# Kernel optimization log

Hardware: AMD Instinct MI355X
Metric: run time of the kernel (lower is better)

## Reference

```python
import jax, jax.numpy as jnp
import numpy as np

B, T, D = 2, 2048, 1024
NH, DH = 16, 64  # inner = NH*DH = D
SCALE_INIT = 0.02


def setup_inputs() -> dict:
    key = jax.random.key(0)
    kx, kq, kk, kv, ko = jax.random.split(key, 5)
    return {
        "x": jax.random.normal(kx, (B, T, D), dtype=jnp.float32),
        "Wq": jax.random.normal(kq, (D, NH * DH), dtype=jnp.float32) * SCALE_INIT,
        "Wk": jax.random.normal(kk, (D, NH * DH), dtype=jnp.float32) * SCALE_INIT,
        "Wv": jax.random.normal(kv, (D, NH * DH), dtype=jnp.float32) * SCALE_INIT,
        "Wo": jax.random.normal(ko, (NH * DH, D), dtype=jnp.float32) * SCALE_INIT,
    }


def reference(x, Wq, Wk, Wv, Wo):
    # x: (B, T, D)
    b, t, _ = x.shape

    def split_heads(h):
        # (B, T, NH*DH) -> (B, NH, T, DH)
        return h.reshape(b, t, NH, DH).transpose(0, 2, 1, 3)

    q = split_heads(x @ Wq)
    k = split_heads(x @ Wk)
    v = split_heads(x @ Wv)

    scale = jnp.asarray(1.0 / np.sqrt(DH), dtype=x.dtype)
    # The per-chunk loop in the original is mathematically equivalent to
    # full causal attention: each query row attends to keys with k_pos <= q_pos.
    scores = jnp.einsum("bhqd,bhkd->bhqk", q, k) * scale  # (B, NH, T, T)
    causal_mask = jnp.arange(t)[None, :] > jnp.arange(t)[:, None]  # k_pos > q_pos
    scores = jnp.where(causal_mask, -jnp.inf, scores)
    attn = jax.nn.softmax(scores, axis=-1)
    attn = jnp.nan_to_num(attn)  # matches torch.nan_to_num (no fully-masked rows in causal case)
    o = jnp.einsum("bhqk,bhkd->bhqd", attn, v)  # (B, NH, T, DH)
    o = o.transpose(0, 2, 1, 3).reshape(b, t, NH * DH)  # merge heads
    return o @ Wo  # (B, T, D)
```

## Files before the change

### kernel.cpp

```cpp
#include <hip/hip_runtime.h>
#include <hip/hip_bf16.h>
#include <string.h>

#define Bsz 2
#define Tsz 2048
#define Dsz 1024
#define NHsz 16
#define Msz (Bsz*Tsz)

typedef unsigned short bfu;
typedef __attribute__((ext_vector_type(8))) short short8;
typedef __attribute__((ext_vector_type(4))) short short4v;
typedef __attribute__((ext_vector_type(4))) float floatx4;

__device__ __forceinline__ bfu f2bf(float f) {
  unsigned int u = __builtin_bit_cast(unsigned int, f);
  u += 0x7fffu + ((u >> 16) & 1u);
  return (bfu)(u >> 16);
}

__device__ __forceinline__ float fexp2(float x) {
#if __has_builtin(__builtin_amdgcn_exp2f)
  return __builtin_amdgcn_exp2f(x);
#else
  return exp2f(x);
#endif
}

__device__ __forceinline__ short4v pack4bf(float a, float b, float c_, float d) {
  __hip_bfloat162 h01 = __float22bfloat162_rn(make_float2(a, b));
  __hip_bfloat162 h23 = __float22bfloat162_rn(make_float2(c_, d));
  uint2 uu;
  memcpy(&uu.x, &h01, 4);
  memcpy(&uu.y, &h23, 4);
  return __builtin_bit_cast(short4v, uu);
}

__device__ __forceinline__ short8 pack8bf(float4 a, float4 b) {
  __hip_bfloat162 h0 = __float22bfloat162_rn(make_float2(a.x, a.y));
  __hip_bfloat162 h1 = __float22bfloat162_rn(make_float2(a.z, a.w));
  __hip_bfloat162 h2 = __float22bfloat162_rn(make_float2(b.x, b.y));
  __hip_bfloat162 h3 = __float22bfloat162_rn(make_float2(b.z, b.w));
  uint4 u;
  memcpy(&u.x, &h0, 4); memcpy(&u.y, &h1, 4);
  memcpy(&u.z, &h2, 4); memcpy(&u.w, &h3, 4);
  return __builtin_bit_cast(short8, u);
}

__device__ __forceinline__ void async16(const void* g, void* l) {
  void* gnc = (void*)g;
  __builtin_amdgcn_global_load_lds((__attribute__((address_space(1))) void*)gnc,
                                   (__attribute__((address_space(3))) void*)l,
                                   16, 0, 0);
}

__global__ __launch_bounds__(256) void transpose_w(const float* __restrict__ W0, const float* __restrict__ W1,
                                                   const float* __restrict__ W2, const float* __restrict__ W3,
                                                   bfu* __restrict__ wt,
                                                   const float* __restrict__ x, bfu* __restrict__ xb) {
  if (blockIdx.z == 4) {
    const int bf = (int)blockIdx.y * 32 + (int)blockIdx.x;
    const size_t i = ((size_t)bf * 256 + threadIdx.y * 32 + threadIdx.x) * 16;
    float4 a0 = *(const float4*)(x + i),     a1 = *(const float4*)(x + i + 4);
    float4 b0 = *(const float4*)(x + i + 8), b1 = *(const float4*)(x + i + 12);
    *(short8*)(xb + i)     = pack8bf(a0, a1);
    *(short8*)(xb + i + 8) = pack8bf(b0, b1);
    return;
  }
  __shared__ float tile[32][33];
  const float* W = blockIdx.z == 0 ? W0 : blockIdx.z == 1 ? W1 : blockIdx.z == 2 ? W2 : W3;
  const float s = (blockIdx.z == 0) ? 0.18033688011112042f : 1.0f;
  bfu* WT = wt + (size_t)blockIdx.z * Dsz * Dsz;
  int tx = threadIdx.x, ty = threadIdx.y;
  int kb = blockIdx.y * 32, nb = blockIdx.x * 32;
#pragma unroll
  for (int i = 0; i < 4; ++i)
    tile[ty + i*8][tx] = W[(size_t)(kb + ty + i*8) * Dsz + nb + tx];
  __syncthreads();
#pragma unroll
  for (int i = 0; i < 4; ++i)
    WT[(size_t)(nb + ty + i*8) * Dsz + kb + tx] = f2bf(tile[tx][ty + i*8] * s);
}

template <bool F32OUT, int NT>
__global__ __launch_bounds__(256) void gemm128(const bfu* __restrict__ Ain, const bfu* __restrict__ Bt0,
                                               void* __restrict__ C0, int K, int N,
                                               size_t strideB, size_t strideC) {
  constexpr int NJ = NT / 32;
  const int tid = threadIdx.x, wave = tid >> 6, lane = tid & 63;
  const int g = lane >> 4, c = lane & 15;
  const int m0 = blockIdx.y * 128, n0 = blockIdx.x * NT;
  const bfu* Bt = Bt0 + strideB * blockIdx.z;
  __shared__ bfu smem[2][4096 + NT * 32];
  floatx4 acc[4][NJ] = {};
  const int srow = lane >> 2;
  const int scol = (((lane & 3) ^ ((lane >> 3) & 3)) << 3);
  const bfu* gB = Bt + (size_t)(n0 + srow) * K + scol;
  const bfu* gA = Ain + (size_t)(m0 + srow) * K + scol;
  const int wm = (wave >> 1) * 64, wn = (wave & 1) * (NT / 2);
  const int roct = (g ^ ((c >> 1) & 3)) << 3;

#define STAGE_G(buf, k0)                                                        \
  {                                                                             \
    _Pragma("unroll")                                                           \
    for (int cc = 0; cc < 2; ++cc) {                                            \
      const int chunk = wave * 2 + cc;                                          \
      async16(gA + (size_t)chunk * 16 * K + (k0), &smem[buf][chunk * 512]);     \
    }                                                                           \
    _Pragma("unroll")                                                           \
    for (int cc = 0; cc < NT / 64; ++cc) {                                      \
      const int chunk = wave * (NT / 64) + cc;                                  \
      async16(gB + (size_t)chunk * 16 * K + (k0), &smem[buf][4096 + chunk * 512]); \
    }                                                                           \
  }

  const int NK = K / 32;
  STAGE_G(0, 0);
  for (int t = 0; t < NK; ++t) {
    const int cur = t & 1;
    if (t + 1 < NK) {
      STAGE_G(cur ^ 1, (t + 1) * 32);
      if (NT == 128) asm volatile("s_waitcnt vmcnt(4)" ::: "memory");
      else           asm volatile("s_waitcnt vmcnt(3)" ::: "memory");
    } else {
      asm volatile("s_waitcnt vmcnt(0)" ::: "memory");
    }
    __builtin_amdgcn_s_barrier();
    asm volatile("" ::: "memory");

    const bfu* AsC = &smem[cur][0];
    const bfu* BsC = &smem[cur][4096];
    short8 afr[4], bfr[NJ];
#pragma unroll
    for (int i = 0; i < 4; ++i) afr[i] = *(const short8*)&AsC[(wm + i*16 + c) * 32 + roct];
#pragma unroll
    for (int j = 0; j < NJ; ++j) bfr[j] = *(const short8*)&BsC[(wn + j*16 + c) * 32 + roct];
#pragma unroll
    for (int i = 0; i < 4; ++i)
#pragma unroll
      for (int j = 0; j < NJ; ++j)
        acc[i][j] = __builtin_amdgcn_mfma_f32_16x16x32_bf16(afr[i], bfr[j], acc[i][j], 0, 0, 0);

    asm volatile("" ::: "memory");
    __builtin_amdgcn_s_barrier();
    asm volatile("" ::: "memory");
  }
#undef STAGE_G

  const bool vtrans = (!F32OUT) && (NT == 128) && (blockIdx.z == 2);
  if (vtrans) {
    bfu* sm = &smem[0][0];
    bfu* vtp = (bfu*)C0 + (size_t)2 * strideC;
#pragma unroll
    for (int p = 0; p < 2; ++p) {
      __syncthreads();
      if ((wave & 1) == p) {
#pragma unroll
        for (int i = 0; i < 4; ++i)
#pragma unroll
          for (int j = 0; j < NJ; ++j) {
            const int nl = j*16 + c;
            const int mg = ((wm + i*16) >> 3) + (g >> 1);
            const int phys = nl * 128 + ((mg ^ (nl & 15)) << 3) + ((g & 1) << 2);
            *(short4v*)&sm[phys] = pack4bf(acc[i][j][0], acc[i][j][1],
                                           acc[i][j][2], acc[i][j][3]);
          }
      }
      __syncthreads();
      const int h_ = (n0 + p * 64) >> 6;
      bfu* dst = vtp + ((size_t)((m0 >> 11) * 16 + h_) * 64) * Tsz + (m0 & 2047);
#pragma unroll
      for (int s = 0; s < 4; ++s) {
        const int nl = s * 16 + (tid >> 4);
        const int me = (tid & 15) << 3;
        const int phys = nl * 128 + (((me >> 3) ^ (nl & 15)) << 3);
        *(short8*)&dst[(size_t)nl * Tsz + me] = *(const short8*)&sm[phys];
      }
    }
    return;
  }

#pragma unroll
  for (int i = 0; i < 4; ++i) {
#pragma unroll
    for (int j = 0; j < NJ; ++j) {
      const int m = m0 + wm + i*16 + g*4;
      const int n = n0 + wn + j*16 + c;
#pragma unroll
      for (int r = 0; r < 4; ++r) {
        float v = acc[i][j][r];
        if (F32OUT) ((float*)C0)[(size_t)(m + r) * N + n] = v;
        else        ((bfu*)C0)[strideC * blockIdx.z + (size_t)(m + r) * N + n] = f2bf(v);
      }
    }
  }
}

__global__ __launch_bounds__(256, 4) void attn_kernel(const bfu* __restrict__ qkv,
                                                      float* __restrict__ op0,
                                                      float* __restrict__ op1,
                                                      float2* __restrict__ ml) {
  const int tid = threadIdx.x, wave = tid >> 6, lane = tid & 63;
  const int g = (lane >> 4) & 3, c = lane & 15, c7 = c & 7;

  const int flat = (int)blockIdx.y * 32 + (int)blockIdx.x;
  const int xcd = flat & 7, r_ = flat >> 3;
  const int ksplit = r_ & 1;
  const int s = (r_ >> 1) & 3, j0 = r_ >> 3;
  const int bh = xcd * 4 + s;
  const int b = bh >> 4, h = bh & 15;

  const size_t hbq = (size_t)b * Tsz * Dsz + h * 64;
  const bfu* Qp = qkv + hbq;
  const bfu* Kp = qkv + (size_t)Msz * Dsz + hbq;
  const bfu* Vt = qkv + (size_t)2 * Msz * Dsz + (size_t)bh * 64 * Tsz;
  float* op = ksplit ? op1 : op0;

  __shared__ bfu Ks[2][64 * 64];
  __shared__ bfu Vs[2][64 * 64];

  const int srow8 = lane >> 3;
  const int soff = ((lane & 7) ^ srow8) << 3;
  const floatx4 z4 = {0.0f, 0.0f, 0.0f, 0.0f};

  for (int hf = 0; hf < 2; ++hf) {
    const int j = hf ? (31 - j0) : j0;
    const int qw = j * 64 + wave * 16;

    short8 bq[2];
#pragma unroll
    for (int kk = 0; kk < 2; ++kk)
      bq[kk] = *(const short8*)(Qp + (size_t)(qw + c) * Dsz + kk * 32 + g * 8);

    floatx4 acc[4] = {};
    float mi = -3.0e38f, li = 0.0f;

    if (ksplit <= j) {
      const bfu* kpp[2]; const bfu* vpp[2];
#pragma unroll
      for (int cc = 0; cc < 2; ++cc) {
        const int ch = wave * 2 + cc;
        kpp[cc] = Kp + (size_t)(ksplit * 64 + ch * 8 + srow8) * Dsz + soff;
        vpp[cc] = Vt + (size_t)(ch * 8 + srow8) * Tsz + ksplit * 64 + soff;
      }

#pragma unroll
      for (int cc = 0; cc < 2; ++cc) {
        const int ch = wave * 2 + cc;
        async16(kpp[cc], &Ks[0][ch * 512]);
        async16(vpp[cc], &Vs[0][ch * 512]);
        kpp[cc] += (size_t)128 * Dsz;
        vpp[cc] += 128;
      }

      int cur = 0;
      for (int kt = ksplit; kt <= j; kt += 2) {
        if (kt + 2 <= j) {
#pragma unroll
          for (int cc = 0; cc < 2; ++cc) {
            const int ch = wave * 2 + cc;
            async16(kpp[cc], &Ks[cur ^ 1][ch * 512]);
            async16(vpp[cc], &Vs[cur ^ 1][ch * 512]);
            kpp[cc] += (size_t)128 * Dsz;
            vpp[cc] += 128;
          }
          asm volatile("s_waitcnt vmcnt(4)" ::: "memory");
        } else {
          asm volatile("s_waitcnt vmcnt(0)" ::: "memory");
        }
        __builtin_amdgcn_s_barrier();
        asm volatile("" ::: "memory");

        const bfu* KsC = &Ks[cur][0];
        const bfu* VsC = &Vs[cur][0];

        floatx4 st[4];
        __builtin_amdgcn_s_setprio(1);
#pragma unroll
        for (int mk = 0; mk < 4; ++mk) {
          const short8 kf = *(const short8*)&KsC[(mk * 16 + c) * 64 + ((g ^ c7) << 3)];
          st[mk] = __builtin_amdgcn_mfma_f32_16x16x32_bf16(kf, bq[0], z4, 0, 0, 0);
        }
#pragma unroll
        for (int mk = 0; mk < 4; ++mk) {
          const short8 kf = *(const short8*)&KsC[(mk * 16 + c) * 64 + (((4 + g) ^ c7) << 3)];
          st[mk] = __builtin_amdgcn_mfma_f32_16x16x32_bf16(kf, bq[1], st[mk], 0, 0, 0);
        }
        __builtin_amdgcn_s_setprio(0);

        if (kt == j) {
#pragma unroll
          for (int mk = 0; mk < 4; ++mk) {
            const int keyb = kt * 64 + mk * 16 + g * 4;
#pragma unroll
            for (int r = 0; r < 4; ++r)
              if (keyb + r > qw + c) st[mk][r] = -1.0e38f;
          }
        }

        float mloc = -3.0e38f;
#pragma unroll
        for (int mk = 0; mk < 4; ++mk)
          mloc = fmaxf(mloc, fmaxf(fmaxf(st[mk][0], st[mk][1]),
                                   fmaxf(st[mk][2], st[mk][3])));
        const bool resc = !__all(mloc <= mi + 8.0f);
        if (resc) {
          float mr = fmaxf(mloc, __shfl_xor(mloc, 16));
          mr = fmaxf(mr, __shfl_xor(mr, 32));
          const float mnew = fmaxf(mi, mr);
          const float alpha = fexp2(mi - mnew);
          li *= alpha;
          mi = mnew;
          float al[4];
#pragma unroll
          for (int rr = 0; rr < 4; ++rr) al[rr] = __shfl(alpha, (lane & 48) | (g * 4 + rr));
#pragma unroll
          for (int nd = 0; nd < 4; ++nd)
#pragma unroll
            for (int rr = 0; rr < 4; ++rr) acc[nd][rr] *= al[rr];
        }
        short4v pa[4];
#pragma unroll
        for (int mk = 0; mk < 4; ++mk) {
          const float p0 = fexp2(st[mk][0] - mi);
          const float p1 = fexp2(st[mk][1] - mi);
          const float p2 = fexp2(st[mk][2] - mi);
          const float p3 = fexp2(st[mk][3] - mi);
          li += (p0 + p1) + (p2 + p3);
          pa[mk] = pack4bf(p0, p1, p2, p3);
        }

        __builtin_amdgcn_s_setprio(1);
#pragma unroll
        for (int mk = 0; mk < 4; ++mk)
#pragma unroll
          for (int nd = 0; nd < 4; ++nd) {
            const short4v vf = *(const short4v*)&VsC[(nd * 16 + c) * 64 +
                ((((mk << 1) + (g >> 1)) ^ c7) << 3) + ((g & 1) << 2)];
            acc[nd] = __builtin_amdgcn_mfma_f32_16x16x16bf16_1k(pa[mk], vf, acc[nd], 0, 0, 0);
          }
        __builtin_amdgcn_s_setprio(0);

        asm volatile("" ::: "memory");
        __builtin_amdgcn_s_barrier();
        asm volatile("" ::: "memory");
        cur ^= 1;
      }
    }

    float lt = li;
    lt += __shfl_xor(lt, 16);
    lt += __shfl_xor(lt, 32);
#pragma unroll
    for (int rr = 0; rr < 4; ++rr) {
      const float lr = __shfl(lt, (lane & 48) | (g * 4 + rr));
      const float inv = lr > 0.0f ? 1.0f / lr : 0.0f;
#pragma unroll
      for (int nd = 0; nd < 4; ++nd)
        op[(size_t)(b * Tsz + qw + g * 4 + rr) * Dsz + h * 64 + nd * 16 + c] =
            acc[nd][rr] * inv;
    }
    if (lane < 16)
      ml[(size_t)ksplit * 65536 + bh * 2048 + qw + c] = make_float2(mi, lt);
  }
}

__global__ __launch_bounds__(256) void merge_split(const float* __restrict__ o0,
                                                   const float* __restrict__ o1,
                                                   const float2* __restrict__ ml,
                                                   bfu* __restrict__ ob) {
  const int idx = blockIdx.x * 256 + threadIdx.x;
  const int row = idx >> 7, ch = idx & 127;
  const int b = row >> 11, q = row & 2047;
  const int bh = b * 16 + (ch >> 3);
  const float2 a0 = ml[bh * 2048 + q];
  const float2 a1 = ml[65536 + bh * 2048 + q];
  const float M = fmaxf(a0.x, a1.x);
  const float w0 = fexp2(a0.x - M) * a0.y;
  const float w1 = fexp2(a1.x - M) * a1.y;
  const float inv = 1.0f / (w0 + w1);
  const float u0 = w0 * inv, u1 = w1 * inv;
  const size_t off = (size_t)row * 1024 + ch * 8;
  float4 p0 = *(const float4*)(o0 + off), q0 = *(const float4*)(o0 + off + 4);
  float4 p1 = *(const float4*)(o1 + off), q1 = *(const float4*)(o1 + off + 4);
  float4 ra, rb;
  ra.x = u0*p0.x + u1*p1.x; ra.y = u0*p0.y + u1*p1.y;
  ra.z = u0*p0.z + u1*p1.z; ra.w = u0*p0.w + u1*p1.w;
  rb.x = u0*q0.x + u1*q1.x; rb.y = u0*q0.y + u1*q1.y;
  rb.z = u0*q0.z + u1*q1.z; rb.w = u0*q0.w + u1*q1.w;
  *(short8*)(ob + off) = pack8bf(ra, rb);
}

extern "C" void kernel_launch(void* const* d_in, const int* in_sizes, int n_in,
                              void* d_out, int out_size, void* d_ws, size_t ws_size,
                              hipStream_t stream) {
  const float* x  = (const float*)d_in[0];
  const float* Wq = (const float*)d_in[1];
  const float* Wk = (const float*)d_in[2];
  const float* Wv = (const float*)d_in[3];
  const float* Wo = (const float*)d_in[4];
  float* out = (float*)d_out;

  bfu* wt    = (bfu*)d_ws;
  bfu* qkv   = wt + (size_t)4 * Dsz * Dsz;
  bfu* obuf  = qkv + (size_t)3 * Msz * Dsz;
  float* op0 = (float*)(obuf + (size_t)Msz * Dsz);
  float* op1 = op0 + (size_t)Msz * Dsz;
  float2* ml = (float2*)(op1 + (size_t)Msz * Dsz);

  transpose_w<<<dim3(32, 32, 5), dim3(32, 8), 0, stream>>>(Wq, Wk, Wv, Wo, wt, x, obuf);
  gemm128<false, 128><<<dim3(Dsz / 128, Msz / 128, 3), dim3(256), 0, stream>>>(
      obuf, wt, (void*)qkv, Dsz, Dsz, (size_t)Dsz * Dsz, (size_t)Msz * Dsz);
  attn_kernel<<<dim3(32, 32), dim3(256), 0, stream>>>(qkv, op0, op1, ml);
  merge_split<<<dim3(2048), dim3(256), 0, stream>>>(op0, op1, ml, obuf);
  gemm128<true, 64><<<dim3(Dsz / 64, Msz / 128, 1), dim3(256), 0, stream>>>(
      obuf, wt + (size_t)3 * Dsz * Dsz, (void*)out, Dsz, Dsz,
      (size_t)0, (size_t)0);
}
```

Baseline: 185.6 us.

## Rework attention to 32x32 MFMA tiles with 4-way key split and fp16 partials

Switches the attention inner loop from 16x16 MFMA tiles to 32x32x16 bf16 MFMA tiles, so each wave now owns 32 query rows. Blocks are remapped to pairs of 128-row query tiles with a 4-way key split instead of 2-way, and waves skip key tiles past their causal limit. Partial outputs are stored as fp16 rather than fp32, and a 4-way merge kernel combines them. The aim is better matrix-core efficiency and less partial-output traffic, at the cost of idle waves inside a block, extra lane shuffles to rebuild the P operand, and fp16 rounding of the partials.

Measured after the change: 231.8 us. 1.25x slower.

```diff
diff --git a/kernel.cpp b/kernel.cpp
--- a/kernel.cpp
+++ b/kernel.cpp
@@ -1,5 +1,6 @@
 #include <hip/hip_runtime.h>
 #include <hip/hip_bf16.h>
+#include <hip/hip_fp16.h>
 #include <string.h>
 
 #define Bsz 2
@@ -12,6 +13,7 @@
 typedef __attribute__((ext_vector_type(8))) short short8;
 typedef __attribute__((ext_vector_type(4))) short short4v;
 typedef __attribute__((ext_vector_type(4))) float floatx4;
+typedef __attribute__((ext_vector_type(16))) float floatx16;
 
 __device__ __forceinline__ bfu f2bf(float f) {
   unsigned int u = __builtin_bit_cast(unsigned int, f);
@@ -27,23 +29,20 @@
 #endif
 }
 
+__device__ __forceinline__ unsigned pkbf(float a, float b) {
+  __hip_bfloat162 t = __float22bfloat162_rn(make_float2(a, b));
+  unsigned u; memcpy(&u, &t, 4); return u;
+}
+
 __device__ __forceinline__ short4v pack4bf(float a, float b, float c_, float d) {
-  __hip_bfloat162 h01 = __float22bfloat162_rn(make_float2(a, b));
-  __hip_bfloat162 h23 = __float22bfloat162_rn(make_float2(c_, d));
-  uint2 uu;
-  memcpy(&uu.x, &h01, 4);
-  memcpy(&uu.y, &h23, 4);
+  uint2 uu; uu.x = pkbf(a, b); uu.y = pkbf(c_, d);
   return __builtin_bit_cast(short4v, uu);
 }
 
 __device__ __forceinline__ short8 pack8bf(float4 a, float4 b) {
-  __hip_bfloat162 h0 = __float22bfloat162_rn(make_float2(a.x, a.y));
-  __hip_bfloat162 h1 = __float22bfloat162_rn(make_float2(a.z, a.w));
-  __hip_bfloat162 h2 = __float22bfloat162_rn(make_float2(b.x, b.y));
-  __hip_bfloat162 h3 = __float22bfloat162_rn(make_float2(b.z, b.w));
   uint4 u;
-  memcpy(&u.x, &h0, 4); memcpy(&u.y, &h1, 4);
-  memcpy(&u.z, &h2, 4); memcpy(&u.w, &h3, 4);
+  u.x = pkbf(a.x, a.y); u.y = pkbf(a.z, a.w);
+  u.z = pkbf(b.x, b.y); u.w = pkbf(b.z, b.w);
   return __builtin_bit_cast(short8, u);
 }
 
@@ -197,72 +196,82 @@
 }
 
 __global__ __launch_bounds__(256, 4) void attn_kernel(const bfu* __restrict__ qkv,
-                                                      float* __restrict__ op0,
-                                                      float* __restrict__ op1,
+                                                      unsigned short* __restrict__ op,
                                                       float2* __restrict__ ml) {
   const int tid = threadIdx.x, wave = tid >> 6, lane = tid & 63;
-  const int g = (lane >> 4) & 3, c = lane & 15, c7 = c & 7;
+  const int l31 = lane & 31, h = lane >> 5, l7 = lane & 7;
 
   const int flat = (int)blockIdx.y * 32 + (int)blockIdx.x;
   const int xcd = flat & 7, r_ = flat >> 3;
-  const int ksplit = r_ & 1;
-  const int s = (r_ >> 1) & 3, j0 = r_ >> 3;
-  const int bh = xcd * 4 + s;
-  const int b = bh >> 4, h = bh & 15;
-
-  const size_t hbq = (size_t)b * Tsz * Dsz + h * 64;
+  const int s_ = r_ & 3, ks = (r_ >> 2) & 3, ap = r_ >> 4;
+  const int bh = xcd * 4 + s_;
+  const int b = bh >> 4, hd = bh & 15;
+
+  const size_t hbq = (size_t)b * Tsz * Dsz + hd * 64;
   const bfu* Qp = qkv + hbq;
   const bfu* Kp = qkv + (size_t)Msz * Dsz + hbq;
   const bfu* Vt = qkv + (size_t)2 * Msz * Dsz + (size_t)bh * 64 * Tsz;
-  float* op = ksplit ? op1 : op0;
 
   __shared__ bfu Ks[2][64 * 64];
   __shared__ bfu Vs[2][64 * 64];
 
   const int srow8 = lane >> 3;
   const int soff = ((lane & 7) ^ srow8) << 3;
-  const floatx4 z4 = {0.0f, 0.0f, 0.0f, 0.0f};
-
-  for (int hf = 0; hf < 2; ++hf) {
-    const int j = hf ? (31 - j0) : j0;
-    const int qw = j * 64 + wave * 16;
-
-    short8 bq[2];
-#pragma unroll
-    for (int kk = 0; kk < 2; ++kk)
-      bq[kk] = *(const short8*)(Qp + (size_t)(qw + c) * Dsz + kk * 32 + g * 8);
-
-    floatx4 acc[4] = {};
+
+  int kfo[2][4], vfo[4][2];
+#pragma unroll
+  for (int kh = 0; kh < 2; ++kh)
+#pragma unroll
+    for (int dc = 0; dc < 4; ++dc)
+      kfo[kh][dc] = (kh*32 + l31)*64 + (((dc*2 + h) ^ l7) << 3);
+#pragma unroll
+  for (int s = 0; s < 4; ++s)
+#pragma unroll
+    for (int db = 0; db < 2; ++db)
+      vfo[s][db] = (db*32 + l31)*64 + (((s*2 + h) ^ l7) << 3);
+
+  for (int sw = 0; sw < 2; ++sw) {
+    const int p = sw ? (15 - ap) : ap;
+    const int ktend = 2*p + 1;
+    const int tq = 2*p + (wave >> 1);
+    const int qw = tq * 64 + (wave & 1) * 32;
+    const int myq = qw + l31;
+
+    floatx16 acc0 = {}, acc1 = {};
     float mi = -3.0e38f, li = 0.0f;
 
-    if (ksplit <= j) {
+    if (ks <= ktend) {
+      short8 bq[4];
+#pragma unroll
+      for (int dc = 0; dc < 4; ++dc)
+        bq[dc] = *(const short8*)(Qp + (size_t)myq * Dsz + dc*16 + h*8);
+
       const bfu* kpp[2]; const bfu* vpp[2];
 #pragma unroll
       for (int cc = 0; cc < 2; ++cc) {
-        const int ch = wave * 2 + cc;
-        kpp[cc] = Kp + (size_t)(ksplit * 64 + ch * 8 + srow8) * Dsz + soff;
-        vpp[cc] = Vt + (size_t)(ch * 8 + srow8) * Tsz + ksplit * 64 + soff;
-      }
-
+        const int ch = wave*2 + cc;
+        kpp[cc] = Kp + (size_t)(ks*64 + ch*8 + srow8) * Dsz + soff;
+        vpp[cc] = Vt + (size_t)(ch*8 + srow8) * Tsz + ks*64 + soff;
+      }
 #pragma unroll
       for (int cc = 0; cc < 2; ++cc) {
-        const int ch = wave * 2 + cc;
-        async16(kpp[cc], &Ks[0][ch * 512]);
-        async16(vpp[cc], &Vs[0][ch * 512]);
-        kpp[cc] += (size_t)128 * Dsz;
-        vpp[cc] += 128;
+        const int ch = wave*2 + cc;
+        async16(kpp[cc], &Ks[0][ch*512]);
+        async16(vpp[cc], &Vs[0][ch*512]);
+        kpp[cc] += (size_t)256 * Dsz;
+        vpp[cc] += 256;
       }
 
       int cur = 0;
-      for (int kt = ksplit; kt <= j; kt += 2) {
-        if (kt + 2 <= j) {
+      for (int kt = ks; kt <= ktend; kt += 4) {
+        if (kt + 4 <= ktend) {
 #pragma unroll
           for (int cc = 0; cc < 2; ++cc) {
-            const int ch = wave * 2 + cc;
-            async16(kpp[cc], &Ks[cur ^ 1][ch * 512]);
-            async16(vpp[cc], &Vs[cur ^ 1][ch * 512]);
-            kpp[cc] += (size_t)128 * Dsz;
-            vpp[cc] += 128;
+            const int ch = wave*2 + cc;
+            async16(kpp[cc], &Ks[cur ^ 1][ch*512]);
+            async16(vpp[cc], &Vs[cur ^ 1][ch*512]);
+            kpp[cc] += (size_t)256 * Dsz;
+            vpp[cc] += 256;
           }
           asm volatile("s_waitcnt vmcnt(4)" ::: "memory");
         } else {
@@ -271,75 +280,84 @@
         __builtin_amdgcn_s_barrier();
         asm volatile("" ::: "memory");
 
-        const bfu* KsC = &Ks[cur][0];
-        const bfu* VsC = &Vs[cur][0];
-
-        floatx4 st[4];
-        __builtin_amdgcn_s_setprio(1);
-#pragma unroll
-        for (int mk = 0; mk < 4; ++mk) {
-          const short8 kf = *(const short8*)&KsC[(mk * 16 + c) * 64 + ((g ^ c7) << 3)];
-          st[mk] = __builtin_amdgcn_mfma_f32_16x16x32_bf16(kf, bq[0], z4, 0, 0, 0);
+        if (kt <= tq) {
+          const bfu* KsC = &Ks[cur][0];
+          const bfu* VsC = &Vs[cur][0];
+
+          floatx16 st0 = {}, st1 = {};
+          __builtin_amdgcn_s_setprio(1);
+#pragma unroll
+          for (int dc = 0; dc < 4; ++dc) {
+            const short8 kf0 = *(const short8*)&KsC[kfo[0][dc]];
+            st0 = __builtin_amdgcn_mfma_f32_32x32x16_bf16(kf0, bq[dc], st0, 0, 0, 0);
+            const short8 kf1 = *(const short8*)&KsC[kfo[1][dc]];
+            st1 = __builtin_amdgcn_mfma_f32_32x32x16_bf16(kf1, bq[dc], st1, 0, 0, 0);
+          }
+          __builtin_amdgcn_s_setprio(0);
+
+          if (kt == tq) {
+#pragma unroll
+            for (int r = 0; r < 16; ++r) {
+              const int k0 = kt*64 + (r & 3) + 8*(r >> 2) + 4*h;
+              if (k0 > myq)      st0[r] = -1.0e38f;
+              if (k0 + 32 > myq) st1[r] = -1.0e38f;
+            }
+          }
+
+          float mx[8];
+#pragma unroll
+          for (int i = 0; i < 8; ++i)
+            mx[i] = fmaxf(fmaxf(st0[2*i], st0[2*i+1]), fmaxf(st1[2*i], st1[2*i+1]));
+          float mloc = fmaxf(fmaxf(fmaxf(mx[0], mx[1]), fmaxf(mx[2], mx[3])),
+                             fmaxf(fmaxf(mx[4], mx[5]), fmaxf(mx[6], mx[7])));
+          const bool resc = !__all(mloc <= mi + 8.0f);
+          if (resc) {
+            const float mr = fmaxf(mloc, __shfl_xor(mloc, 32));
+            const float mnew = fmaxf(mi, mr);
+            const float alpha = fexp2(mi - mnew);
+            li *= alpha; mi = mnew;
+#pragma unroll
+            for (int r = 0; r < 16; ++r) {
+              const float al = __shfl(alpha, (r & 3) + 8*(r >> 2) + 4*h);
+              acc0[r] *= al; acc1[r] *= al;
+            }
+          }
+          float sum = 0.0f;
+#pragma unroll
+          for (int r = 0; r < 16; ++r) { st0[r] = fexp2(st0[r] - mi); sum += st0[r]; }
+#pragma unroll
+          for (int r = 0; r < 16; ++r) { st1[r] = fexp2(st1[r] - mi); sum += st1[r]; }
+          li += sum;
+
+          __builtin_amdgcn_s_setprio(1);
+#pragma unroll
+          for (int s = 0; s < 4; ++s) {
+            const int base = 8 * (s & 1);
+            unsigned w0, w1, w2, w3;
+            if (s < 2) {
+              w0 = pkbf(st0[base],   st0[base+1]); w1 = pkbf(st0[base+2], st0[base+3]);
+              w2 = pkbf(st0[base+4], st0[base+5]); w3 = pkbf(st0[base+6], st0[base+7]);
+            } else {
+              w0 = pkbf(st1[base],   st1[base+1]); w1 = pkbf(st1[base+2], st1[base+3]);
+              w2 = pkbf(st1[base+4], st1[base+5]); w3 = pkbf(st1[base+6], st1[base+7]);
+            }
+            const unsigned w0x = (unsigned)__shfl_xor((int)w0, 32);
+            const unsigned w1x = (unsigned)__shfl_xor((int)w1, 32);
+            const unsigned w2x = (unsigned)__shfl_xor((int)w2, 32);
+            const unsigned w3x = (unsigned)__shfl_xor((int)w3, 32);
+            uint4 au;
+            au.x = h ? w2x : w0;
+            au.y = h ? w3x : w1;
+            au.z = h ? w2  : w0x;
+            au.w = h ? w3  : w1x;
+            const short8 pa = __builtin_bit_cast(short8, au);
+            const short8 vf0 = *(const short8*)&VsC[vfo[s][0]];
+            acc0 = __builtin_amdgcn_mfma_f32_32x32x16_bf16(pa, vf0, acc0, 0, 0, 0);
+            const short8 vf1 = *(const short8*)&VsC[vfo[s][1]];
+            acc1 = __builtin_amdgcn_mfma_f32_32x32x16_bf16(pa, vf1, acc1, 0, 0, 0);
+          }
+          __builtin_amdgcn_s_setprio(0);
         }
-#pragma unroll
-        for (int mk = 0; mk < 4; ++mk) {
-          const short8 kf = *(const short8*)&KsC[(mk * 16 + c) * 64 + (((4 + g) ^ c7) << 3)];
-          st[mk] = __builtin_amdgcn_mfma_f32_16x16x32_bf16(kf, bq[1], st[mk], 0, 0, 0);
-        }
-        __builtin_amdgcn_s_setprio(0);
-
-        if (kt == j) {
-#pragma unroll
-          for (int mk = 0; mk < 4; ++mk) {
-            const int keyb = kt * 64 + mk * 16 + g * 4;
-#pragma unroll
-            for (int r = 0; r < 4; ++r)
-              if (keyb + r > qw + c) st[mk][r] = -1.0e38f;
-          }
-        }
-
-        float mloc = -3.0e38f;
-#pragma unroll
-        for (int mk = 0; mk < 4; ++mk)
-          mloc = fmaxf(mloc, fmaxf(fmaxf(st[mk][0], st[mk][1]),
-                                   fmaxf(st[mk][2], st[mk][3])));
-        const bool resc = !__all(mloc <= mi + 8.0f);
-        if (resc) {
-          float mr = fmaxf(mloc, __shfl_xor(mloc, 16));
-          mr = fmaxf(mr, __shfl_xor(mr, 32));
-          const float mnew = fmaxf(mi, mr);
-          const float alpha = fexp2(mi - mnew);
-          li *= alpha;
-          mi = mnew;
-          float al[4];
-#pragma unroll
-          for (int rr = 0; rr < 4; ++rr) al[rr] = __shfl(alpha, (lane & 48) | (g * 4 + rr));
-#pragma unroll
-          for (int nd = 0; nd < 4; ++nd)
-#pragma unroll
-            for (int rr = 0; rr < 4; ++rr) acc[nd][rr] *= al[rr];
-        }
-        short4v pa[4];
-#pragma unroll
-        for (int mk = 0; mk < 4; ++mk) {
-          const float p0 = fexp2(st[mk][0] - mi);
-          const float p1 = fexp2(st[mk][1] - mi);
-          const float p2 = fexp2(st[mk][2] - mi);
-          const float p3 = fexp2(st[mk][3] - mi);
-          li += (p0 + p1) + (p2 + p3);
-          pa[mk] = pack4bf(p0, p1, p2, p3);
-        }
-
-        __builtin_amdgcn_s_setprio(1);
-#pragma unroll
-        for (int mk = 0; mk < 4; ++mk)
-#pragma unroll
-          for (int nd = 0; nd < 4; ++nd) {
-            const short4v vf = *(const short4v*)&VsC[(nd * 16 + c) * 64 +
-                ((((mk << 1) + (g >> 1)) ^ c7) << 3) + ((g & 1) << 2)];
-            acc[nd] = __builtin_amdgcn_mfma_f32_16x16x16bf16_1k(pa[mk], vf, acc[nd], 0, 0, 0);
-          }
-        __builtin_amdgcn_s_setprio(0);
 
         asm volatile("" ::: "memory");
         __builtin_amdgcn_s_barrier();
@@ -348,46 +366,53 @@
       }
     }
 
-    float lt = li;
-    lt += __shfl_xor(lt, 16);
-    lt += __shfl_xor(lt, 32);
-#pragma unroll
-    for (int rr = 0; rr < 4; ++rr) {
-      const float lr = __shfl(lt, (lane & 48) | (g * 4 + rr));
-      const float inv = lr > 0.0f ? 1.0f / lr : 0.0f;
-#pragma unroll
-      for (int nd = 0; nd < 4; ++nd)
-        op[(size_t)(b * Tsz + qw + g * 4 + rr) * Dsz + h * 64 + nd * 16 + c] =
-            acc[nd][rr] * inv;
-    }
-    if (lane < 16)
-      ml[(size_t)ksplit * 65536 + bh * 2048 + qw + c] = make_float2(mi, lt);
-  }
-}
-
-__global__ __launch_bounds__(256) void merge_split(const float* __restrict__ o0,
-                                                   const float* __restrict__ o1,
-                                                   const float2* __restrict__ ml,
-                                                   bfu* __restrict__ ob) {
+    const float lt = li + __shfl_xor(li, 32);
+    const float invq = lt > 0.0f ? 1.0f / lt : 0.0f;
+    __half* oph = (__half*)op + (size_t)ks * Msz * Dsz;
+#pragma unroll
+    for (int r = 0; r < 16; ++r) {
+      const int qr = (r & 3) + 8*(r >> 2) + 4*h;
+      const float iv = __shfl(invq, qr);
+      const size_t rowo = (size_t)(b * Tsz + qw + qr) * Dsz + hd * 64 + l31;
+      oph[rowo]      = __float2half_rn(acc0[r] * iv);
+      oph[rowo + 32] = __float2half_rn(acc1[r] * iv);
+    }
+    if (lane < 32)
+      ml[(size_t)ks * 65536 + bh * 2048 + qw + l31] = make_float2(mi, lt);
+  }
+}
+
+__global__ __launch_bounds__(256) void merge4(const unsigned short* __restrict__ op,
+                                              const float2* __restrict__ ml,
+                                              bfu* __restrict__ ob) {
   const int idx = blockIdx.x * 256 + threadIdx.x;
   const int row = idx >> 7, ch = idx & 127;
   const int b = row >> 11, q = row & 2047;
   const int bh = b * 16 + (ch >> 3);
-  const float2 a0 = ml[bh * 2048 + q];
-  const float2 a1 = ml[65536 + bh * 2048 + q];
-  const float M = fmaxf(a0.x, a1.x);
-  const float w0 = fexp2(a0.x - M) * a0.y;
-  const float w1 = fexp2(a1.x - M) * a1.y;
-  const float inv = 1.0f / (w0 + w1);
-  const float u0 = w0 * inv, u1 = w1 * inv;
+  float2 a[4]; float M = -3.0e38f;
+#pragma unroll
+  for (int s = 0; s < 4; ++s) {
+    a[s] = ml[(size_t)s * 65536 + bh * 2048 + q];
+    M = fmaxf(M, a[s].x);
+  }
+  float w[4], tw = 0.0f;
+#pragma unroll
+  for (int s = 0; s < 4; ++s) { w[s] = fexp2(a[s].x - M) * a[s].y; tw += w[s]; }
+  const float inv = 1.0f / tw;
   const size_t off = (size_t)row * 1024 + ch * 8;
-  float4 p0 = *(const float4*)(o0 + off), q0 = *(const float4*)(o0 + off + 4);
-  float4 p1 = *(const float4*)(o1 + off), q1 = *(const float4*)(o1 + off + 4);
-  float4 ra, rb;
-  ra.x = u0*p0.x + u1*p1.x; ra.y = u0*p0.y + u1*p1.y;
-  ra.z = u0*p0.z + u1*p1.z; ra.w = u0*p0.w + u1*p1.w;
-  rb.x = u0*q0.x + u1*q1.x; rb.y = u0*q0.y + u1*q1.y;
-  rb.z = u0*q0.z + u1*q1.z; rb.w = u0*q0.w + u1*q1.w;
+  float o[8] = {};
+#pragma unroll
+  for (int s = 0; s < 4; ++s) {
+    const float u = w[s] * inv;
+    const __half2* ph = (const __half2*)(op + (size_t)s * Msz * Dsz + off);
+#pragma unroll
+    for (int e = 0; e < 4; ++e) {
+      const float2 f = __half22float2(ph[e]);
+      o[2*e]   += u * f.x;
+      o[2*e+1] += u * f.y;
+    }
+  }
+  float4 ra = {o[0], o[1], o[2], o[3]}, rb = {o[4], o[5], o[6], o[7]};
   *(short8*)(ob + off) = pack8bf(ra, rb);
 }
 
@@ -404,15 +429,14 @@
   bfu* wt    = (bfu*)d_ws;
   bfu* qkv   = wt + (size_t)4 * Dsz * Dsz;
   bfu* obuf  = qkv + (size_t)3 * Msz * Dsz;
-  float* op0 = (float*)(obuf + (size_t)Msz * Dsz);
-  float* op1 = op0 + (size_t)Msz * Dsz;
-  float2* ml = (float2*)(op1 + (size_t)Msz * Dsz);
+  unsigned short* op = (unsigned short*)(obuf + (size_t)Msz * Dsz);
+  float2* ml = (float2*)(op + (size_t)4 * Msz * Dsz);
 
   transpose_w<<<dim3(32, 32, 5), dim3(32, 8), 0, stream>>>(Wq, Wk, Wv, Wo, wt, x, obuf);
   gemm128<false, 128><<<dim3(Dsz / 128, Msz / 128, 3), dim3(256), 0, stream>>>(
       obuf, wt, (void*)qkv, Dsz, Dsz, (size_t)Dsz * Dsz, (size_t)Msz * Dsz);
-  attn_kernel<<<dim3(32, 32), dim3(256), 0, stream>>>(qkv, op0, op1, ml);
-  merge_split<<<dim3(2048), dim3(256), 0, stream>>>(op0, op1, ml, obuf);
+  attn_kernel<<<dim3(32, 32), dim3(256), 0, stream>>>(qkv, op, ml);
+  merge4<<<dim3(2048), dim3(256), 0, stream>>>(op, ml, obuf);
   gemm128<true, 64><<<dim3(Dsz / 64, Msz / 128, 1), dim3(256), 0, stream>>>(
       obuf, wt + (size_t)3 * Dsz * Dsz, (void*)out, Dsz, Dsz,
       (size_t)0, (size_t)0);
```
